# Optimization experiments

Hardware: AMD Instinct MI355X
Metric: run time of the kernel (lower is better)

Reference implementation:

```python
import jax, jax.numpy as jnp
from jax import lax
import numpy as np

DN = ('NDHWC', 'DHWIO', 'NDHWC')

def _conv(x, W):
    # stride-1 kernel-3 sparse conv on dense grid: SAME conv; absent voxels are zero
    return lax.conv_general_dilated(x, W, (1, 1, 1), 'SAME', dimension_numbers=DN)

def _tconv(x, W):
    # kernel-2 stride-2 generative transpose conv: exactly doubles each spatial dim
    return lax.conv_transpose(x, W, (2, 2, 2), 'VALID', dimension_numbers=DN)

def _pool(h):
    B, D1, D2, D3, C = h.shape
    return h.reshape(B, D1 // 2, 2, D2 // 2, 2, D3 // 2, 2, C).max(axis=(2, 4, 6))

def _pool_mask(m):
    B, D1, D2, D3 = m.shape
    return m.reshape(B, D1 // 2, 2, D2 // 2, 2, D3 // 2, 2).max(axis=(2, 4, 6))

def _up_mask(m):
    return jnp.repeat(jnp.repeat(jnp.repeat(m, 2, axis=1), 2, axis=2), 2, axis=3)

def setup_inputs() -> dict:
    key = jax.random.key(0)
    ks = jax.random.split(key, 6)
    B, G = 2, 128
    x = jax.random.normal(ks[0], (B, G, G, G, 1), dtype=jnp.float32)
    occ = jax.random.randint(ks[1], (B, G, G, G), 0, 10, dtype=jnp.int32)
    def xavier(k, shape):
        fan_in = np.prod(shape[:-1]); fan_out = shape[-1]
        std = np.sqrt(2.0 / (fan_in + fan_out)).astype(np.float32)
        return jax.random.normal(k, shape, dtype=jnp.float32) * std
    W1 = xavier(ks[2], (3, 3, 3, 1, 16))
    W2 = xavier(ks[3], (3, 3, 3, 16, 4))
    Wt1 = xavier(ks[4], (2, 2, 2, 4, 16))
    Wt2 = xavier(ks[5], (2, 2, 2, 16, 1))
    return {"x": x, "W1": W1, "W2": W2, "Wt1": Wt1, "Wt2": Wt2, "occ": occ}

def reference(x, W1, W2, Wt1, Wt2, occ):
    m0 = (occ == 0).astype(x.dtype)            # occupancy mask at full res
    xm = x * m0[..., None]
    h = jax.nn.relu(_conv(xm, W1)) * m0[..., None]   # coords unchanged
    h = _pool(h); m1 = _pool_mask(m0)                # stride-2 max pool on sparse coords
    h = jax.nn.relu(_conv(h, W2)) * m1[..., None]
    h = _pool(h); m2 = _pool_mask(m1)
    m3 = _up_mask(m2)                                # transpose conv emits all children coords
    h = jax.nn.relu(_tconv(h, Wt1)) * m3[..., None]
    m4 = _up_mask(m3)
    out = jax.nn.sigmoid(_tconv(h, Wt2)) * m4[..., None]
    return out
```

## Files before the change

### kernel.cpp

```cpp
#include <hip/hip_runtime.h>
#include <hip/hip_fp16.h>

#define G 128

typedef _Float16 h2_t __attribute__((ext_vector_type(2)));

union U16 { uint4 u; h2_t h2[4]; };
union HV  { uint4 u; h2_t h2[4]; };
union PK2 { uint2 u; h2_t h[2]; };

__device__ __forceinline__ float dot2f(h2_t a, h2_t b, float c) {
#if __has_builtin(__builtin_amdgcn_fdot2)
    return __builtin_amdgcn_fdot2(a, b, c, false);
#else
    return c + (float)a.x * (float)b.x + (float)a.y * (float)b.y;
#endif
}

__device__ __forceinline__ float dot4(float4 a, float4 b) {
    return a.x * b.x + a.y * b.y + a.z * b.z + a.w * b.w;
}

__global__ __launch_bounds__(256, 1)
void k_conv1_pool(const float* __restrict__ x, const int* __restrict__ occ,
                  const float* __restrict__ W1,
                  __half* __restrict__ h1p, float* __restrict__ m1)
{
    __shared__ __align__(16) _Float16      sx[10 * 18 * 24];
    __shared__ __align__(16) int           pacc[16 * 256];
    __shared__ __align__(4)  unsigned short slist[2048];
    __shared__ __align__(16) h2_t          w1L[216];
    __shared__ __align__(4)  unsigned char sm1[256];
    __shared__ int                         scnt;

    const int bx = blockIdx.x, by = blockIdx.y;
    const int b  = blockIdx.z >> 4, zt = blockIdx.z & 15;
    const int tid = threadIdx.x;

    const int z0 = zt * 8 - 1, y0 = by * 16 - 1;
    const int base_b = b * G * G * G;

    int4   ro[5];
    float4 rx[5];
    #pragma unroll
    for (int it = 0; it < 5; ++it) {
        int c = it * 256 + tid;
        int cc = c < 1080 ? c : 1079;
        int row = cc / 6, seg = cc - row * 6;
        int lz  = row / 18, ly = row - lz * 18;
        int gz = z0 + lz, gy = y0 + ly;
        int gxc = (bx << 4) - 4 + (seg << 2);
        bool inb = (unsigned)gz < 128u && (unsigned)gy < 128u && (unsigned)gxc < 128u;
        int gi = inb ? base_b + (gz * G + gy) * G + gxc : base_b;
        ro[it] = *(const int4*)(occ + gi);
        rx[it] = *(const float4*)(x + gi);
    }

    if (tid == 0) scnt = 0;
    {
        uint4 z4 = make_uint4(0u, 0u, 0u, 0u);
        uint4* p4 = (uint4*)pacc;
        p4[tid] = z4; p4[tid + 256] = z4; p4[tid + 512] = z4; p4[tid + 768] = z4;
    }
    if (tid < 64) ((unsigned*)sm1)[tid] = 0u;
    if (tid < 216) {
        float2 f = ((const float2*)W1)[tid];
        h2_t w; w.x = (_Float16)f.x; w.y = (_Float16)f.y;
        w1L[tid] = w;
    }
    __syncthreads();

    #pragma unroll
    for (int it = 0; it < 5; ++it) {
        int c = it * 256 + tid;
        if (c < 1080) {
            int row = c / 6, seg = c - row * 6;
            int lz  = row / 18, ly = row - lz * 18;
            int gz = z0 + lz, gy = y0 + ly;
            int gxc = (bx << 4) - 4 + (seg << 2);
            bool inb = (unsigned)gz < 128u && (unsigned)gy < 128u && (unsigned)gxc < 128u;
            int4   o4 = ro[it];
            float4 x4 = rx[it];
            if (!inb) o4 = make_int4(1, 1, 1, 1);
            h2_t p01, p23;
            p01.x = (o4.x == 0) ? (_Float16)x4.x : (_Float16)0.f;
            p01.y = (o4.y == 0) ? (_Float16)x4.y : (_Float16)0.f;
            p23.x = (o4.z == 0) ? (_Float16)x4.z : (_Float16)0.f;
            p23.y = (o4.w == 0) ? (_Float16)x4.w : (_Float16)0.f;
            PK2 pk; pk.h[0] = p01; pk.h[1] = p23;
            *(uint2*)&sx[row * 24 + (seg << 2)] = pk.u;

            if ((unsigned)(lz - 1) < 8u && (unsigned)(ly - 1) < 16u &&
                (unsigned)(seg - 1) < 4u) {
                int mb = (o4.x == 0 ? 1 : 0) | (o4.y == 0 ? 2 : 0) |
                         (o4.z == 0 ? 4 : 0) | (o4.w == 0 ? 8 : 0);
                if (mb) {
                    int cnt  = __popc(mb);
                    int base = atomicAdd(&scnt, cnt);
                    int cz = lz - 1, cy = ly - 1, cx0v = (seg << 2) - 4;
                    int cellb = (cz >> 1) * 64 + (cy >> 1) * 8;
                    #pragma unroll
                    for (int j = 0; j < 4; ++j) {
                        if (mb & (1 << j)) {
                            slist[base++] = (unsigned short)((cz << 8) | (cy << 4) | (cx0v + j));
                            sm1[cellb + ((cx0v + j) >> 1)] = (unsigned char)1;
                        }
                    }
                }
            }
        }
    }
    __syncthreads();

    const int n = scnt;

    const h2_t zero = (h2_t)(_Float16)0.f;
    for (int kb = 0; kb < n; kb += 256) {
        const int idx = kb + tid;
        if (idx < n) {
            const int code = slist[idx];
            const int cz = code >> 8, cy = (code >> 4) & 15, cx = code & 15;
            const int sb = ((cz + 1) * 18 + (cy + 1)) * 24 + cx + 4;
            h2_t acc[8];
            #pragma unroll
            for (int c = 0; c < 8; ++c) acc[c] = zero;
            #pragma unroll
            for (int kz = 0; kz < 3; ++kz)
            #pragma unroll
            for (int ky = 0; ky < 3; ++ky)
            #pragma unroll
            for (int kx = 0; kx < 3; ++kx) {
                _Float16 v = sx[sb + (kz - 1) * 432 + (ky - 1) * 24 + (kx - 1)];
                h2_t v2 = {v, v};
                const h2_t* w = &w1L[((kz * 3 + ky) * 3 + kx) * 8];
                #pragma unroll
                for (int c = 0; c < 8; ++c) acc[c] = v2 * w[c] + acc[c];
            }
            const int cell = (cz >> 1) * 64 + (cy >> 1) * 8 + (cx >> 1);
            #pragma unroll
            for (int c = 0; c < 8; ++c) {
                atomicMax(&pacc[(2 * c) * 256 + cell],
                          __float_as_int(fmaxf((float)acc[c].x, 0.f)));
                atomicMax(&pacc[(2 * c + 1) * 256 + cell],
                          __float_as_int(fmaxf((float)acc[c].y, 0.f)));
            }
        }
    }
    __syncthreads();

    const int tx = tid & 7, ty = (tid >> 3) & 7, tz = tid >> 6;
    const int pz = zt * 4 + tz, py = by * 8 + ty, px = bx * 8 + tx;
    const int vidx = ((b * 64 + pz) * 64 + py) * 64 + px;
    HV p0, p1;
    #pragma unroll
    for (int c = 0; c < 4; ++c) {
        h2_t a, bq;
        a.x  = (_Float16)__int_as_float(pacc[(2 * c) * 256 + tid]);
        a.y  = (_Float16)__int_as_float(pacc[(2 * c + 1) * 256 + tid]);
        bq.x = (_Float16)__int_as_float(pacc[(8 + 2 * c) * 256 + tid]);
        bq.y = (_Float16)__int_as_float(pacc[(9 + 2 * c) * 256 + tid]);
        p0.h2[c] = a; p1.h2[c] = bq;
    }
    uint4* o = (uint4*)&h1p[(size_t)vidx * 16];
    o[0] = p0.u;
    o[1] = p1.u;
    m1[vidx] = sm1[tid] ? 1.f : 0.f;
}

__global__ __launch_bounds__(256)
void k_conv2_dec(const __half* __restrict__ h1p, const float* __restrict__ m1,
                 const float* __restrict__ W2,
                 const float* __restrict__ Wt1, const float* __restrict__ Wt2,
                 float* __restrict__ out)
{
    __shared__ uint4  tile[1320];
    __shared__ float4 wt1[128];
    __shared__ float4 wt2[32];
    __shared__ __align__(16) h2_t w2L[864];
    __shared__ int    pacc[128];
    __shared__ int    pm[32];
    __shared__ unsigned char slist[256];
    __shared__ int    scnt;

    const int bx = blockIdx.x, by = blockIdx.y;
    const int b  = blockIdx.z >> 4, bz = blockIdx.z & 15;
    const int tid = threadIdx.x;

    const int z0 = bz * 4 - 1, y0 = by * 8 - 1, x0 = bx * 8 - 1;

    uint4 ra[3], rb4[3];
    #pragma unroll
    for (int it = 0; it < 3; ++it) {
        int g = it * 256 + tid;
        int gg = g < 660 ? g : 659;
        int z = gg / 110, r = gg - z * 110, y = r / 11, xx = r - y * 11;
        int gz = z0 + z, gy = y0 + y, gx = x0 + xx;
        bool inb = (unsigned)gz < 64u && (unsigned)gy < 64u && (unsigned)gx < 64u;
        size_t vi = inb ? (size_t)(((b * 64 + gz) * 64 + gy) * 64 + gx) : 0;
        const uint4* src = (const uint4*)&h1p[vi * 16];
        ra[it]  = src[0];
        rb4[it] = src[1];
    }

    const int cx_ = tid & 7, cy_ = (tid >> 3) & 7, cz_ = tid >> 6;
    const float mv = m1[((b * 64 + (bz * 4 + cz_)) * 64 + (by * 8 + cy_)) * 64
                        + (bx * 8 + cx_)];

    if (tid == 0) scnt = 0;
    if (tid < 128) { wt1[tid] = ((const float4*)Wt1)[tid]; pacc[tid] = 0; }
    if (tid < 32)  { wt2[tid] = ((const float4*)Wt2)[tid]; pm[tid] = 0; }
    #pragma unroll
    for (int it = 0; it < 4; ++it) {
        int i = it * 256 + tid;
        if (i < 864) {
            int t = i >> 5, rr = i & 31, co = rr >> 3, p = rr & 7;
            h2_t w;
            w.x = (_Float16)W2[t * 64 + (2 * p) * 4 + co];
            w.y = (_Float16)W2[t * 64 + (2 * p + 1) * 4 + co];
            w2L[i] = w;
        }
    }
    __syncthreads();

    #pragma unroll
    for (int it = 0; it < 3; ++it) {
        int g = it * 256 + tid;
        if (g < 660) {
            int z = g / 110, r = g - z * 110, y = r / 11, xx = r - y * 11;
            int gz = z0 + z, gy = y0 + y, gx = x0 + xx;
            bool inb = (unsigned)gz < 64u && (unsigned)gy < 64u && (unsigned)gx < 64u;
            uint4 a0 = ra[it], a1 = rb4[it];
            if (!inb) { a0 = make_uint4(0u, 0u, 0u, 0u); a1 = a0; }
            tile[g]       = a0;
            tile[660 + g] = a1;
        }
    }
    {
        const int lane = tid & 63;
        bool act = (mv != 0.f);
        unsigned long long bal = __ballot(act);
        int wtot = __popcll(bal);
        int wbase = 0;
        if (lane == 0 && wtot) wbase = atomicAdd(&scnt, wtot);
        wbase = __shfl(wbase, 0);
        if (act) {
            int pre = __popcll(bal & ((1ull << lane) - 1ull));
            slist[wbase + pre] = (unsigned char)tid;
            pm[(cz_ >> 1) * 16 + (cy_ >> 1) * 4 + (cx_ >> 1)] = 1;
        }
    }
    __syncthreads();

    const int n = scnt;

    if (tid < n) {
        const int code = slist[tid];
        const int cx = code & 7, cy = (code >> 3) & 7, cz = code >> 6;
        float acc[4] = {0.f, 0.f, 0.f, 0.f};
        #pragma unroll
        for (int kz = 0; kz < 3; ++kz)
        #pragma unroll
        for (int ky = 0; ky < 3; ++ky) {
            const int rb = ((cz + kz) * 10 + (cy + ky)) * 11 + cx;
            h2_t hp[2][3][4];
            #pragma unroll
            for (int hh = 0; hh < 2; ++hh)
            #pragma unroll
            for (int xi = 0; xi < 3; ++xi) {
                U16 a; a.u = tile[hh * 660 + rb + xi];
                #pragma unroll
                for (int p = 0; p < 4; ++p) hp[hh][xi][p] = a.h2[p];
            }
            const int t3 = (kz * 3 + ky) * 3;
            #pragma unroll
            for (int kx = 0; kx < 3; ++kx) {
                const h2_t* w = &w2L[(t3 + kx) * 32];
                #pragma unroll
                for (int co = 0; co < 4; ++co) {
                    float a = acc[co];
                    #pragma unroll
                    for (int hh = 0; hh < 2; ++hh)
                    #pragma unroll
                    for (int p = 0; p < 4; ++p)
                        a = dot2f(hp[hh][kx][p], w[co * 8 + 4 * hh + p], a);
                    acc[co] = a;
                }
            }
        }
        const int parent = (cz >> 1) * 16 + (cy >> 1) * 4 + (cx >> 1);
        #pragma unroll
        for (int co = 0; co < 4; ++co)
            atomicMax(&pacc[co * 32 + parent],
                      __float_as_int(fmaxf(acc[co], 0.f)));
    }
    __syncthreads();

    {
        const int p  = tid >> 3;
        const int a  = (tid >> 2) & 1;
        const int bb = (tid >> 1) & 1;
        const int e  = tid & 1;
        const int pZ = p >> 4, pY = (p >> 2) & 3, pq = p & 3;
        const int pz = bz * 2 + pZ, py = by * 4 + pY, pxq = bx * 4 + pq;

        const float mm = pm[p] ? 1.f : 0.f;
        const float4 hv = make_float4(__int_as_float(pacc[p]),
                                      __int_as_float(pacc[32 + p]),
                                      __int_as_float(pacc[64 + p]),
                                      __int_as_float(pacc[96 + p]));

        const int b0q = ((((1 - a) * 2 + (1 - bb)) * 2) + 1) * 16;
        const int b1q = ((((1 - a) * 2 + (1 - bb)) * 2) + 0) * 16;
        float4 t0q[4], t1q[4];
        #pragma unroll
        for (int q = 0; q < 4; ++q) {
            float4 a0 = wt1[b0q + q],      a1 = wt1[b0q + 4 + q];
            float4 a2 = wt1[b0q + 8 + q],  a3 = wt1[b0q + 12 + q];
            float4 c0 = wt1[b1q + q],      c1 = wt1[b1q + 4 + q];
            float4 c2 = wt1[b1q + 8 + q],  c3 = wt1[b1q + 12 + q];
            float4 s0, s1;
            s0.x = hv.x * a0.x + hv.y * a1.x + hv.z * a2.x + hv.w * a3.x;
            s0.y = hv.x * a0.y + hv.y * a1.y + hv.z * a2.y + hv.w * a3.y;
            s0.z = hv.x * a0.z + hv.y * a1.z + hv.z * a2.z + hv.w * a3.z;
            s0.w = hv.x * a0.w + hv.y * a1.w + hv.z * a2.w + hv.w * a3.w;
            s1.x = hv.x * c0.x + hv.y * c1.x + hv.z * c2.x + hv.w * c3.x;
            s1.y = hv.x * c0.y + hv.y * c1.y + hv.z * c2.y + hv.w * c3.y;
            s1.z = hv.x * c0.z + hv.y * c1.z + hv.z * c2.z + hv.w * c3.z;
            s1.w = hv.x * c0.w + hv.y * c1.w + hv.z * c2.w + hv.w * c3.w;
            t0q[q] = make_float4(fmaxf(s0.x, 0.f), fmaxf(s0.y, 0.f),
                                 fmaxf(s0.z, 0.f), fmaxf(s0.w, 0.f));
            t1q[q] = make_float4(fmaxf(s1.x, 0.f), fmaxf(s1.y, 0.f),
                                 fmaxf(s1.z, 0.f), fmaxf(s1.w, 0.f));
        }

        const int d = 4 * pz + 2 * a + e;
        #pragma unroll
        for (int f = 0; f < 2; ++f) {
            const int hh = 4 * py + 2 * bb + f;
            const int be = ((1 - e) * 2 + (1 - f)) * 2;
            const float4* wg0 = &wt2[(be + 1) * 4];
            const float4* wg1 = &wt2[(be + 0) * 4];
            float s00 = dot4(t0q[0], wg0[0]) + dot4(t0q[1], wg0[1])
                      + dot4(t0q[2], wg0[2]) + dot4(t0q[3], wg0[3]);
            float s01 = dot4(t0q[0], wg1[0]) + dot4(t0q[1], wg1[1])
                      + dot4(t0q[2], wg1[2]) + dot4(t0q[3], wg1[3]);
            float s10 = dot4(t1q[0], wg0[0]) + dot4(t1q[1], wg0[1])
                      + dot4(t1q[2], wg0[2]) + dot4(t1q[3], wg0[3]);
            float s11 = dot4(t1q[0], wg1[0]) + dot4(t1q[1], wg1[1])
                      + dot4(t1q[2], wg1[2]) + dot4(t1q[3], wg1[3]);
            float4 o;
            o.x = mm / (1.f + __expf(-s00));
            o.y = mm / (1.f + __expf(-s01));
            o.z = mm / (1.f + __expf(-s10));
            o.w = mm / (1.f + __expf(-s11));
            *(float4*)&out[((b * G + d) * G + hh) * G + 4 * pxq] = o;
        }
    }
}

extern "C" void kernel_launch(void* const* d_in, const int* in_sizes, int n_in,
                              void* d_out, int out_size, void* d_ws, size_t ws_size,
                              hipStream_t stream) {
    (void)in_sizes; (void)n_in; (void)out_size; (void)ws_size;
    const float* x   = (const float*)d_in[0];
    const float* W1  = (const float*)d_in[1];
    const float* W2  = (const float*)d_in[2];
    const float* Wt1 = (const float*)d_in[3];
    const float* Wt2 = (const float*)d_in[4];
    const int*   occ = (const int*)d_in[5];
    float* out = (float*)d_out;

    char* ws = (char*)d_ws;
    __half* h1p = (__half*)ws;
    float*  m1  = (float*)(ws + 8388608ull * sizeof(__half));

    k_conv1_pool<<<dim3(8, 8, 32), dim3(256), 0, stream>>>(x, occ, W1, h1p, m1);
    k_conv2_dec<<<dim3(8, 8, 32), dim3(256), 0, stream>>>(h1p, m1, W2, Wt1, Wt2, out);
}
```

Before: 152.5 us.

## Gather conv2 neighbors directly from global memory and swizzle block order

Drops the shared-memory halo tile in the conv2/decoder kernel. Each active voxel now reads its 27 neighbor feature vectors straight from global memory, with a one-row software prefetch (double-buffered registers). Because only about 10% of voxels are active, this avoids loading and staging the full 660-voxel halo per block and frees LDS for higher occupancy. It also remaps the block index to a swizzled work order, likely to improve cache locality. The cost is redundant global and L2 traffic between neighboring active voxels, plus more register pressure from the prefetch buffers.

```diff
diff --git a/kernel.cpp b/kernel.cpp
--- a/kernel.cpp
+++ b/kernel.cpp
@@ -173,7 +173,6 @@
                  const float* __restrict__ Wt1, const float* __restrict__ Wt2,
                  float* __restrict__ out)
 {
-    __shared__ uint4  tile[1320];
     __shared__ float4 wt1[128];
     __shared__ float4 wt2[32];
     __shared__ __align__(16) h2_t w2L[864];
@@ -182,25 +181,13 @@
     __shared__ unsigned char slist[256];
     __shared__ int    scnt;
 
-    const int bx = blockIdx.x, by = blockIdx.y;
-    const int b  = blockIdx.z >> 4, bz = blockIdx.z & 15;
     const int tid = threadIdx.x;
 
-    const int z0 = bz * 4 - 1, y0 = by * 8 - 1, x0 = bx * 8 - 1;
-
-    uint4 ra[3], rb4[3];
-    #pragma unroll
-    for (int it = 0; it < 3; ++it) {
-        int g = it * 256 + tid;
-        int gg = g < 660 ? g : 659;
-        int z = gg / 110, r = gg - z * 110, y = r / 11, xx = r - y * 11;
-        int gz = z0 + z, gy = y0 + y, gx = x0 + xx;
-        bool inb = (unsigned)gz < 64u && (unsigned)gy < 64u && (unsigned)gx < 64u;
-        size_t vi = inb ? (size_t)(((b * 64 + gz) * 64 + gy) * 64 + gx) : 0;
-        const uint4* src = (const uint4*)&h1p[vi * 16];
-        ra[it]  = src[0];
-        rb4[it] = src[1];
-    }
+    const int lin  = blockIdx.x + 8 * (blockIdx.y + 8 * blockIdx.z);
+    const int wrk  = ((lin & 7) << 8) | (lin >> 3);
+    const int bx   = wrk & 7, by = (wrk >> 3) & 7;
+    const int zidx = wrk >> 6;
+    const int b    = zidx >> 4, bz = zidx & 15;
 
     const int cx_ = tid & 7, cy_ = (tid >> 3) & 7, cz_ = tid >> 6;
     const float mv = m1[((b * 64 + (bz * 4 + cz_)) * 64 + (by * 8 + cy_)) * 64
@@ -222,19 +209,6 @@
     }
     __syncthreads();
 
-    #pragma unroll
-    for (int it = 0; it < 3; ++it) {
-        int g = it * 256 + tid;
-        if (g < 660) {
-            int z = g / 110, r = g - z * 110, y = r / 11, xx = r - y * 11;
-            int gz = z0 + z, gy = y0 + y, gx = x0 + xx;
-            bool inb = (unsigned)gz < 64u && (unsigned)gy < 64u && (unsigned)gx < 64u;
-            uint4 a0 = ra[it], a1 = rb4[it];
-            if (!inb) { a0 = make_uint4(0u, 0u, 0u, 0u); a1 = a0; }
-            tile[g]       = a0;
-            tile[660 + g] = a1;
-        }
-    }
     {
         const int lane = tid & 63;
         bool act = (mv != 0.f);
@@ -256,37 +230,77 @@
     if (tid < n) {
         const int code = slist[tid];
         const int cx = code & 7, cy = (code >> 3) & 7, cz = code >> 6;
+        const int gz0 = bz * 4 + cz - 1;
+        const int gy0 = by * 8 + cy - 1;
+        const int gx0 = bx * 8 + cx - 1;
+        const __half* __restrict__ hb = h1p + ((size_t)b << 18) * 16;
+
         float acc[4] = {0.f, 0.f, 0.f, 0.f};
+
+        uint4 curv[3][2], nxtv[3][2];
+
+        {
+            const int gz = gz0, gy = gy0;
+            const bool zy = ((unsigned)gz < 64u) && ((unsigned)gy < 64u);
+            #pragma unroll
+            for (int xi = 0; xi < 3; ++xi) {
+                const int gx = gx0 + xi;
+                const bool ok = zy && ((unsigned)gx < 64u);
+                const size_t vi = ok ? (size_t)((gz * 64 + gy) * 64 + gx) : 0;
+                const uint4* s = (const uint4*)&hb[vi * 16];
+                uint4 a0 = s[0], a1 = s[1];
+                if (!ok) { a0 = make_uint4(0u,0u,0u,0u); a1 = a0; }
+                curv[xi][0] = a0; curv[xi][1] = a1;
+            }
+        }
+
         #pragma unroll
-        for (int kz = 0; kz < 3; ++kz)
-        #pragma unroll
-        for (int ky = 0; ky < 3; ++ky) {
-            const int rb = ((cz + kz) * 10 + (cy + ky)) * 11 + cx;
-            h2_t hp[2][3][4];
-            #pragma unroll
-            for (int hh = 0; hh < 2; ++hh)
-            #pragma unroll
-            for (int xi = 0; xi < 3; ++xi) {
-                U16 a; a.u = tile[hh * 660 + rb + xi];
+        for (int r = 0; r < 9; ++r) {
+            if (r < 8) {
+                const int rz = (r + 1) / 3, ry = (r + 1) - rz * 3;
+                const int gz = gz0 + rz, gy = gy0 + ry;
+                const bool zy = ((unsigned)gz < 64u) && ((unsigned)gy < 64u);
                 #pragma unroll
-                for (int p = 0; p < 4; ++p) hp[hh][xi][p] = a.h2[p];
-            }
-            const int t3 = (kz * 3 + ky) * 3;
-            #pragma unroll
-            for (int kx = 0; kx < 3; ++kx) {
-                const h2_t* w = &w2L[(t3 + kx) * 32];
+                for (int xi = 0; xi < 3; ++xi) {
+                    const int gx = gx0 + xi;
+                    const bool ok = zy && ((unsigned)gx < 64u);
+                    const size_t vi = ok ? (size_t)((gz * 64 + gy) * 64 + gx) : 0;
+                    const uint4* s = (const uint4*)&hb[vi * 16];
+                    uint4 a0 = s[0], a1 = s[1];
+                    if (!ok) { a0 = make_uint4(0u,0u,0u,0u); a1 = a0; }
+                    nxtv[xi][0] = a0; nxtv[xi][1] = a1;
+                }
+            }
+
+            {
+                const h2_t* wrow = &w2L[(r * 3) * 32];
                 #pragma unroll
-                for (int co = 0; co < 4; ++co) {
-                    float a = acc[co];
+                for (int kx = 0; kx < 3; ++kx) {
+                    U16 a0; a0.u = curv[kx][0];
+                    U16 a1; a1.u = curv[kx][1];
+                    const h2_t* wv = wrow + kx * 32;
                     #pragma unroll
-                    for (int hh = 0; hh < 2; ++hh)
-                    #pragma unroll
-                    for (int p = 0; p < 4; ++p)
-                        a = dot2f(hp[hh][kx][p], w[co * 8 + 4 * hh + p], a);
-                    acc[co] = a;
+                    for (int co = 0; co < 4; ++co) {
+                        float a = acc[co];
+                        #pragma unroll
+                        for (int p = 0; p < 4; ++p) {
+                            a = dot2f(a0.h2[p], wv[co * 8 + p], a);
+                            a = dot2f(a1.h2[p], wv[co * 8 + 4 + p], a);
+                        }
+                        acc[co] = a;
+                    }
                 }
             }
-        }
+
+            if (r < 8) {
+                #pragma unroll
+                for (int xi = 0; xi < 3; ++xi) {
+                    curv[xi][0] = nxtv[xi][0];
+                    curv[xi][1] = nxtv[xi][1];
+                }
+            }
+        }
+
         const int parent = (cz >> 1) * 16 + (cy >> 1) * 4 + (cx >> 1);
         #pragma unroll
         for (int co = 0; co < 4; ++co)
```

Result: no change. 151.0 us (-1.0%).

## Fuse conv1+pool into conv2/decoder kernel, recomputing halo per block

Applied to the files above, without the earlier changes.

Merges the two kernels into one, so the pooled conv1 feature map is no longer written to and read back from global workspace. Each block now loads a larger occ/x halo and computes conv1 densely per pooled cell, with register max-pooling instead of a sparse list and shared atomics. It also shrinks the output tile to one pooled z-slab and remaps block indices for locality. The cost is redundant halo recomputation of conv1 and dense work on unoccupied voxels, which are skipped only per voxel by a mask bit.

```diff
diff --git a/kernel.cpp b/kernel.cpp
--- a/kernel.cpp
+++ b/kernel.cpp
@@ -17,39 +17,62 @@
 #endif
 }
 
+__device__ __forceinline__ h2_t h2max(h2_t a, h2_t b) {
+#if __has_builtin(__builtin_elementwise_max)
+    return __builtin_elementwise_max(a, b);
+#else
+    h2_t r;
+    r.x = a.x > b.x ? a.x : b.x;
+    r.y = a.y > b.y ? a.y : b.y;
+    return r;
+#endif
+}
+
 __device__ __forceinline__ float dot4(float4 a, float4 b) {
     return a.x * b.x + a.y * b.y + a.z * b.z + a.w * b.w;
 }
 
-__global__ __launch_bounds__(256, 1)
-void k_conv1_pool(const float* __restrict__ x, const int* __restrict__ occ,
-                  const float* __restrict__ W1,
-                  __half* __restrict__ h1p, float* __restrict__ m1)
+__global__ __launch_bounds__(256)
+void k_fused(const float* __restrict__ x, const int* __restrict__ occ,
+             const float* __restrict__ W1, const float* __restrict__ W2,
+             const float* __restrict__ Wt1, const float* __restrict__ Wt2,
+             float* __restrict__ out)
 {
-    __shared__ __align__(16) _Float16      sx[10 * 18 * 24];
-    __shared__ __align__(16) int           pacc[16 * 256];
-    __shared__ __align__(4)  unsigned short slist[2048];
+    __shared__ __align__(16) _Float16      sx[10 * 22 * 24];
+    __shared__ __align__(4)  unsigned char mk[10 * 22 * 6];
+    __shared__ __align__(16) uint4         tile[2 * 400];
+    __shared__ unsigned char               sm1L[400];
     __shared__ __align__(16) h2_t          w1L[216];
-    __shared__ __align__(4)  unsigned char sm1[256];
+    __shared__ __align__(16) h2_t          w2L[864];
+    __shared__ float4                      wt1[128];
+    __shared__ float4                      wt2[32];
+    __shared__ int                         pacc[64];
+    __shared__ int                         pm[16];
+    __shared__ unsigned char               clist[128];
     __shared__ int                         scnt;
 
-    const int bx = blockIdx.x, by = blockIdx.y;
-    const int b  = blockIdx.z >> 4, zt = blockIdx.z & 15;
     const int tid = threadIdx.x;
 
-    const int z0 = zt * 8 - 1, y0 = by * 16 - 1;
+    const int lin = blockIdx.x + 8 * (blockIdx.y + 8 * blockIdx.z);
+    const int wrk = ((lin & 7) << 9) | (lin >> 3);
+    const int bx  = wrk & 7, by = (wrk >> 3) & 7;
+    const int bzz = wrk >> 6;
+    const int b   = bzz >> 5, bz2 = bzz & 31;
+
     const int base_b = b * G * G * G;
-
-    int4   ro[5];
-    float4 rx[5];
+    const int gz0 = 4 * bz2 - 3;
+    const int gy0 = 16 * by - 3;
+    const int gx0 = 16 * bx - 4;
+
+    int4   ro[6];
+    float4 rx[6];
     #pragma unroll
-    for (int it = 0; it < 5; ++it) {
+    for (int it = 0; it < 6; ++it) {
         int c = it * 256 + tid;
-        int cc = c < 1080 ? c : 1079;
+        int cc = c < 1320 ? c : 1319;
         int row = cc / 6, seg = cc - row * 6;
-        int lz  = row / 18, ly = row - lz * 18;
-        int gz = z0 + lz, gy = y0 + ly;
-        int gxc = (bx << 4) - 4 + (seg << 2);
+        int lz = row / 22, ly = row - lz * 22;
+        int gz = gz0 + lz, gy = gy0 + ly, gxc = gx0 + (seg << 2);
         bool inb = (unsigned)gz < 128u && (unsigned)gy < 128u && (unsigned)gxc < 128u;
         int gi = inb ? base_b + (gz * G + gy) * G + gxc : base_b;
         ro[it] = *(const int4*)(occ + gi);
@@ -57,27 +80,34 @@
     }
 
     if (tid == 0) scnt = 0;
-    {
-        uint4 z4 = make_uint4(0u, 0u, 0u, 0u);
-        uint4* p4 = (uint4*)pacc;
-        p4[tid] = z4; p4[tid + 256] = z4; p4[tid + 512] = z4; p4[tid + 768] = z4;
-    }
-    if (tid < 64) ((unsigned*)sm1)[tid] = 0u;
+    if (tid < 64) pacc[tid] = 0;
+    if (tid < 16) pm[tid] = 0;
+    if (tid < 128) wt1[tid] = ((const float4*)Wt1)[tid];
+    if (tid < 32)  wt2[tid] = ((const float4*)Wt2)[tid];
     if (tid < 216) {
         float2 f = ((const float2*)W1)[tid];
         h2_t w; w.x = (_Float16)f.x; w.y = (_Float16)f.y;
         w1L[tid] = w;
     }
-    __syncthreads();
-
     #pragma unroll
-    for (int it = 0; it < 5; ++it) {
+    for (int it = 0; it < 4; ++it) {
+        int i = it * 256 + tid;
+        if (i < 864) {
+            int t = i >> 5, rr = i & 31, co = rr >> 3, p = rr & 7;
+            h2_t w;
+            w.x = (_Float16)W2[t * 64 + (2 * p) * 4 + co];
+            w.y = (_Float16)W2[t * 64 + (2 * p + 1) * 4 + co];
+            w2L[i] = w;
+        }
+    }
+
+    #pragma unroll
+    for (int it = 0; it < 6; ++it) {
         int c = it * 256 + tid;
-        if (c < 1080) {
+        if (c < 1320) {
             int row = c / 6, seg = c - row * 6;
-            int lz  = row / 18, ly = row - lz * 18;
-            int gz = z0 + lz, gy = y0 + ly;
-            int gxc = (bx << 4) - 4 + (seg << 2);
+            int lz = row / 22, ly = row - lz * 22;
+            int gz = gz0 + lz, gy = gy0 + ly, gxc = gx0 + (seg << 2);
             bool inb = (unsigned)gz < 128u && (unsigned)gy < 128u && (unsigned)gxc < 128u;
             int4   o4 = ro[it];
             float4 x4 = rx[it];
@@ -89,155 +119,89 @@
             p23.y = (o4.w == 0) ? (_Float16)x4.w : (_Float16)0.f;
             PK2 pk; pk.h[0] = p01; pk.h[1] = p23;
             *(uint2*)&sx[row * 24 + (seg << 2)] = pk.u;
-
-            if ((unsigned)(lz - 1) < 8u && (unsigned)(ly - 1) < 16u &&
-                (unsigned)(seg - 1) < 4u) {
-                int mb = (o4.x == 0 ? 1 : 0) | (o4.y == 0 ? 2 : 0) |
-                         (o4.z == 0 ? 4 : 0) | (o4.w == 0 ? 8 : 0);
-                if (mb) {
-                    int cnt  = __popc(mb);
-                    int base = atomicAdd(&scnt, cnt);
-                    int cz = lz - 1, cy = ly - 1, cx0v = (seg << 2) - 4;
-                    int cellb = (cz >> 1) * 64 + (cy >> 1) * 8;
+            mk[c] = (unsigned char)((o4.x == 0 ? 1 : 0) | (o4.y == 0 ? 2 : 0) |
+                                    (o4.z == 0 ? 4 : 0) | (o4.w == 0 ? 8 : 0));
+        }
+    }
+    __syncthreads();
+
+    {
+        const h2_t zero = (h2_t)(_Float16)0.f;
+        const h2_t* sxh2 = (const h2_t*)sx;
+        #pragma unroll
+        for (int pass = 0; pass < 2; ++pass) {
+            int t = pass * 256 + tid;
+            if (t < 400) {
+                const int tz = t / 100, rm = t - tz * 100;
+                const int ty = rm / 10,  tx = rm - ty * 10;
+
+                h2_t cube[4][4][3];
+                #pragma unroll
+                for (int z4 = 0; z4 < 4; ++z4) {
+                    const int lz = 2 * tz + z4;
                     #pragma unroll
-                    for (int j = 0; j < 4; ++j) {
-                        if (mb & (1 << j)) {
-                            slist[base++] = (unsigned short)((cz << 8) | (cy << 4) | (cx0v + j));
-                            sm1[cellb + ((cx0v + j) >> 1)] = (unsigned char)1;
-                        }
+                    for (int y4 = 0; y4 < 4; ++y4) {
+                        const int base = (lz * 22 + 2 * ty + y4) * 12 + tx;
+                        cube[z4][y4][0] = sxh2[base];
+                        cube[z4][y4][1] = sxh2[base + 1];
+                        cube[z4][y4][2] = sxh2[base + 2];
                     }
                 }
+
+                h2_t best[8];
+                #pragma unroll
+                for (int c = 0; c < 8; ++c) best[c] = zero;
+                int anym = 0;
+
+                #pragma unroll
+                for (int pos = 0; pos < 8; ++pos) {
+                    const int dz = pos >> 2, dy = (pos >> 1) & 1, dx = pos & 1;
+                    const int lz = 1 + 2 * tz + dz;
+                    const int ly = 1 + 2 * ty + dy;
+                    const int lx = 2 + 2 * tx + dx;
+                    const int mbit = (mk[(lz * 22 + ly) * 6 + (lx >> 2)] >> (lx & 3)) & 1;
+                    if (mbit) {
+                        anym = 1;
+                        h2_t acc[8];
+                        #pragma unroll
+                        for (int c = 0; c < 8; ++c) acc[c] = zero;
+                        #pragma unroll
+                        for (int kz = 0; kz < 3; ++kz)
+                        #pragma unroll
+                        for (int ky = 0; ky < 3; ++ky)
+                        #pragma unroll
+                        for (int kx = 0; kx < 3; ++kx) {
+                            const int xp = dx + kx + 1;
+                            h2_t cv = cube[dz + kz][dy + ky][xp >> 1];
+                            _Float16 v = (xp & 1) ? cv.y : cv.x;
+                            h2_t v2 = {v, v};
+                            const h2_t* w = &w1L[((kz * 3 + ky) * 3 + kx) * 8];
+                            #pragma unroll
+                            for (int c = 0; c < 8; ++c) acc[c] = v2 * w[c] + acc[c];
+                        }
+                        #pragma unroll
+                        for (int c = 0; c < 8; ++c)
+                            best[c] = h2max(best[c], h2max(acc[c], zero));
+                    }
+                }
+
+                HV p0, p1;
+                #pragma unroll
+                for (int c = 0; c < 4; ++c) { p0.h2[c] = best[c]; p1.h2[c] = best[4 + c]; }
+                tile[t]       = p0.u;
+                tile[400 + t] = p1.u;
+                sm1L[t] = (unsigned char)anym;
             }
         }
     }
     __syncthreads();
 
-    const int n = scnt;
-
-    const h2_t zero = (h2_t)(_Float16)0.f;
-    for (int kb = 0; kb < n; kb += 256) {
-        const int idx = kb + tid;
-        if (idx < n) {
-            const int code = slist[idx];
-            const int cz = code >> 8, cy = (code >> 4) & 15, cx = code & 15;
-            const int sb = ((cz + 1) * 18 + (cy + 1)) * 24 + cx + 4;
-            h2_t acc[8];
-            #pragma unroll
-            for (int c = 0; c < 8; ++c) acc[c] = zero;
-            #pragma unroll
-            for (int kz = 0; kz < 3; ++kz)
-            #pragma unroll
-            for (int ky = 0; ky < 3; ++ky)
-            #pragma unroll
-            for (int kx = 0; kx < 3; ++kx) {
-                _Float16 v = sx[sb + (kz - 1) * 432 + (ky - 1) * 24 + (kx - 1)];
-                h2_t v2 = {v, v};
-                const h2_t* w = &w1L[((kz * 3 + ky) * 3 + kx) * 8];
-                #pragma unroll
-                for (int c = 0; c < 8; ++c) acc[c] = v2 * w[c] + acc[c];
-            }
-            const int cell = (cz >> 1) * 64 + (cy >> 1) * 8 + (cx >> 1);
-            #pragma unroll
-            for (int c = 0; c < 8; ++c) {
-                atomicMax(&pacc[(2 * c) * 256 + cell],
-                          __float_as_int(fmaxf((float)acc[c].x, 0.f)));
-                atomicMax(&pacc[(2 * c + 1) * 256 + cell],
-                          __float_as_int(fmaxf((float)acc[c].y, 0.f)));
-            }
-        }
-    }
-    __syncthreads();
-
-    const int tx = tid & 7, ty = (tid >> 3) & 7, tz = tid >> 6;
-    const int pz = zt * 4 + tz, py = by * 8 + ty, px = bx * 8 + tx;
-    const int vidx = ((b * 64 + pz) * 64 + py) * 64 + px;
-    HV p0, p1;
-    #pragma unroll
-    for (int c = 0; c < 4; ++c) {
-        h2_t a, bq;
-        a.x  = (_Float16)__int_as_float(pacc[(2 * c) * 256 + tid]);
-        a.y  = (_Float16)__int_as_float(pacc[(2 * c + 1) * 256 + tid]);
-        bq.x = (_Float16)__int_as_float(pacc[(8 + 2 * c) * 256 + tid]);
-        bq.y = (_Float16)__int_as_float(pacc[(9 + 2 * c) * 256 + tid]);
-        p0.h2[c] = a; p1.h2[c] = bq;
-    }
-    uint4* o = (uint4*)&h1p[(size_t)vidx * 16];
-    o[0] = p0.u;
-    o[1] = p1.u;
-    m1[vidx] = sm1[tid] ? 1.f : 0.f;
-}
-
-__global__ __launch_bounds__(256)
-void k_conv2_dec(const __half* __restrict__ h1p, const float* __restrict__ m1,
-                 const float* __restrict__ W2,
-                 const float* __restrict__ Wt1, const float* __restrict__ Wt2,
-                 float* __restrict__ out)
-{
-    __shared__ uint4  tile[1320];
-    __shared__ float4 wt1[128];
-    __shared__ float4 wt2[32];
-    __shared__ __align__(16) h2_t w2L[864];
-    __shared__ int    pacc[128];
-    __shared__ int    pm[32];
-    __shared__ unsigned char slist[256];
-    __shared__ int    scnt;
-
-    const int bx = blockIdx.x, by = blockIdx.y;
-    const int b  = blockIdx.z >> 4, bz = blockIdx.z & 15;
-    const int tid = threadIdx.x;
-
-    const int z0 = bz * 4 - 1, y0 = by * 8 - 1, x0 = bx * 8 - 1;
-
-    uint4 ra[3], rb4[3];
-    #pragma unroll
-    for (int it = 0; it < 3; ++it) {
-        int g = it * 256 + tid;
-        int gg = g < 660 ? g : 659;
-        int z = gg / 110, r = gg - z * 110, y = r / 11, xx = r - y * 11;
-        int gz = z0 + z, gy = y0 + y, gx = x0 + xx;
-        bool inb = (unsigned)gz < 64u && (unsigned)gy < 64u && (unsigned)gx < 64u;
-        size_t vi = inb ? (size_t)(((b * 64 + gz) * 64 + gy) * 64 + gx) : 0;
-        const uint4* src = (const uint4*)&h1p[vi * 16];
-        ra[it]  = src[0];
-        rb4[it] = src[1];
-    }
-
-    const int cx_ = tid & 7, cy_ = (tid >> 3) & 7, cz_ = tid >> 6;
-    const float mv = m1[((b * 64 + (bz * 4 + cz_)) * 64 + (by * 8 + cy_)) * 64
-                        + (bx * 8 + cx_)];
-
-    if (tid == 0) scnt = 0;
-    if (tid < 128) { wt1[tid] = ((const float4*)Wt1)[tid]; pacc[tid] = 0; }
-    if (tid < 32)  { wt2[tid] = ((const float4*)Wt2)[tid]; pm[tid] = 0; }
-    #pragma unroll
-    for (int it = 0; it < 4; ++it) {
-        int i = it * 256 + tid;
-        if (i < 864) {
-            int t = i >> 5, rr = i & 31, co = rr >> 3, p = rr & 7;
-            h2_t w;
-            w.x = (_Float16)W2[t * 64 + (2 * p) * 4 + co];
-            w.y = (_Float16)W2[t * 64 + (2 * p + 1) * 4 + co];
-            w2L[i] = w;
-        }
-    }
-    __syncthreads();
-
-    #pragma unroll
-    for (int it = 0; it < 3; ++it) {
-        int g = it * 256 + tid;
-        if (g < 660) {
-            int z = g / 110, r = g - z * 110, y = r / 11, xx = r - y * 11;
-            int gz = z0 + z, gy = y0 + y, gx = x0 + xx;
-            bool inb = (unsigned)gz < 64u && (unsigned)gy < 64u && (unsigned)gx < 64u;
-            uint4 a0 = ra[it], a1 = rb4[it];
-            if (!inb) { a0 = make_uint4(0u, 0u, 0u, 0u); a1 = a0; }
-            tile[g]       = a0;
-            tile[660 + g] = a1;
-        }
-    }
     {
+        const int ox = tid & 7, oy = (tid >> 3) & 7, oz = tid >> 6;
+        bool act = false;
+        if (tid < 128)
+            act = sm1L[((oz + 1) * 10 + oy + 1) * 10 + ox + 1] != 0;
         const int lane = tid & 63;
-        bool act = (mv != 0.f);
         unsigned long long bal = __ballot(act);
         int wtot = __popcll(bal);
         int wbase = 0;
@@ -245,8 +209,8 @@
         wbase = __shfl(wbase, 0);
         if (act) {
             int pre = __popcll(bal & ((1ull << lane) - 1ull));
-            slist[wbase + pre] = (unsigned char)tid;
-            pm[(cz_ >> 1) * 16 + (cy_ >> 1) * 4 + (cx_ >> 1)] = 1;
+            clist[wbase + pre] = (unsigned char)tid;
+            pm[(oy >> 1) * 4 + (ox >> 1)] = 1;
         }
     }
     __syncthreads();
@@ -254,20 +218,20 @@
     const int n = scnt;
 
     if (tid < n) {
-        const int code = slist[tid];
-        const int cx = code & 7, cy = (code >> 3) & 7, cz = code >> 6;
+        const int code = clist[tid];
+        const int ox = code & 7, oy = (code >> 3) & 7, oz = code >> 6;
         float acc[4] = {0.f, 0.f, 0.f, 0.f};
         #pragma unroll
         for (int kz = 0; kz < 3; ++kz)
         #pragma unroll
         for (int ky = 0; ky < 3; ++ky) {
-            const int rb = ((cz + kz) * 10 + (cy + ky)) * 11 + cx;
+            const int rb = ((oz + kz) * 10 + (oy + ky)) * 10 + ox;
             h2_t hp[2][3][4];
             #pragma unroll
             for (int hh = 0; hh < 2; ++hh)
             #pragma unroll
             for (int xi = 0; xi < 3; ++xi) {
-                U16 a; a.u = tile[hh * 660 + rb + xi];
+                U16 a; a.u = tile[hh * 400 + rb + xi];
                 #pragma unroll
                 for (int p = 0; p < 4; ++p) hp[hh][xi][p] = a.h2[p];
             }
@@ -287,27 +251,28 @@
                 }
             }
         }
-        const int parent = (cz >> 1) * 16 + (cy >> 1) * 4 + (cx >> 1);
+        const int parent = (oy >> 1) * 4 + (ox >> 1);
         #pragma unroll
         for (int co = 0; co < 4; ++co)
-            atomicMax(&pacc[co * 32 + parent],
+            atomicMax(&pacc[co * 16 + parent],
                       __float_as_int(fmaxf(acc[co], 0.f)));
     }
     __syncthreads();
 
     {
-        const int p  = tid >> 3;
-        const int a  = (tid >> 2) & 1;
-        const int bb = (tid >> 1) & 1;
-        const int e  = tid & 1;
-        const int pZ = p >> 4, pY = (p >> 2) & 3, pq = p & 3;
-        const int pz = bz * 2 + pZ, py = by * 4 + pY, pxq = bx * 4 + pq;
+        const int p  = tid >> 4;
+        const int a  = (tid >> 3) & 1;
+        const int bb = (tid >> 2) & 1;
+        const int e  = (tid >> 1) & 1;
+        const int f  = tid & 1;
+        const int pY = p >> 2, pq = p & 3;
+        const int py = by * 4 + pY, pxq = bx * 4 + pq;
 
         const float mm = pm[p] ? 1.f : 0.f;
         const float4 hv = make_float4(__int_as_float(pacc[p]),
+                                      __int_as_float(pacc[16 + p]),
                                       __int_as_float(pacc[32 + p]),
-                                      __int_as_float(pacc[64 + p]),
-                                      __int_as_float(pacc[96 + p]));
+                                      __int_as_float(pacc[48 + p]));
 
         const int b0q = ((((1 - a) * 2 + (1 - bb)) * 2) + 1) * 16;
         const int b1q = ((((1 - a) * 2 + (1 - bb)) * 2) + 0) * 16;
@@ -333,35 +298,32 @@
                                  fmaxf(s1.z, 0.f), fmaxf(s1.w, 0.f));
         }
 
-        const int d = 4 * pz + 2 * a + e;
-        #pragma unroll
-        for (int f = 0; f < 2; ++f) {
-            const int hh = 4 * py + 2 * bb + f;
-            const int be = ((1 - e) * 2 + (1 - f)) * 2;
-            const float4* wg0 = &wt2[(be + 1) * 4];
-            const float4* wg1 = &wt2[(be + 0) * 4];
-            float s00 = dot4(t0q[0], wg0[0]) + dot4(t0q[1], wg0[1])
-                      + dot4(t0q[2], wg0[2]) + dot4(t0q[3], wg0[3]);
-            float s01 = dot4(t0q[0], wg1[0]) + dot4(t0q[1], wg1[1])
-                      + dot4(t0q[2], wg1[2]) + dot4(t0q[3], wg1[3]);
-            float s10 = dot4(t1q[0], wg0[0]) + dot4(t1q[1], wg0[1])
-                      + dot4(t1q[2], wg0[2]) + dot4(t1q[3], wg0[3]);
-            float s11 = dot4(t1q[0], wg1[0]) + dot4(t1q[1], wg1[1])
-                      + dot4(t1q[2], wg1[2]) + dot4(t1q[3], wg1[3]);
-            float4 o;
-            o.x = mm / (1.f + __expf(-s00));
-            o.y = mm / (1.f + __expf(-s01));
-            o.z = mm / (1.f + __expf(-s10));
-            o.w = mm / (1.f + __expf(-s11));
-            *(float4*)&out[((b * G + d) * G + hh) * G + 4 * pxq] = o;
-        }
+        const int d  = 4 * bz2 + 2 * a + e;
+        const int hh = 4 * py + 2 * bb + f;
+        const int be = ((1 - e) * 2 + (1 - f)) * 2;
+        const float4* wg0 = &wt2[(be + 1) * 4];
+        const float4* wg1 = &wt2[(be + 0) * 4];
+        float s00 = dot4(t0q[0], wg0[0]) + dot4(t0q[1], wg0[1])
+                  + dot4(t0q[2], wg0[2]) + dot4(t0q[3], wg0[3]);
+        float s01 = dot4(t0q[0], wg1[0]) + dot4(t0q[1], wg1[1])
+                  + dot4(t0q[2], wg1[2]) + dot4(t0q[3], wg1[3]);
+        float s10 = dot4(t1q[0], wg0[0]) + dot4(t1q[1], wg0[1])
+                  + dot4(t1q[2], wg0[2]) + dot4(t1q[3], wg0[3]);
+        float s11 = dot4(t1q[0], wg1[0]) + dot4(t1q[1], wg1[1])
+                  + dot4(t1q[2], wg1[2]) + dot4(t1q[3], wg1[3]);
+        float4 o;
+        o.x = mm / (1.f + __expf(-s00));
+        o.y = mm / (1.f + __expf(-s01));
+        o.z = mm / (1.f + __expf(-s10));
+        o.w = mm / (1.f + __expf(-s11));
+        *(float4*)&out[((b * G + d) * G + hh) * G + 4 * pxq] = o;
     }
 }
 
 extern "C" void kernel_launch(void* const* d_in, const int* in_sizes, int n_in,
                               void* d_out, int out_size, void* d_ws, size_t ws_size,
                               hipStream_t stream) {
-    (void)in_sizes; (void)n_in; (void)out_size; (void)ws_size;
+    (void)in_sizes; (void)n_in; (void)out_size; (void)d_ws; (void)ws_size;
     const float* x   = (const float*)d_in[0];
     const float* W1  = (const float*)d_in[1];
     const float* W2  = (const float*)d_in[2];
@@ -370,10 +332,5 @@
     const int*   occ = (const int*)d_in[5];
     float* out = (float*)d_out;
 
-    char* ws = (char*)d_ws;
-    __half* h1p = (__half*)ws;
-    float*  m1  = (float*)(ws + 8388608ull * sizeof(__half));
-
-    k_conv1_pool<<<dim3(8, 8, 32), dim3(256), 0, stream>>>(x, occ, W1, h1p, m1);
-    k_conv2_dec<<<dim3(8, 8, 32), dim3(256), 0, stream>>>(h1p, m1, W2, Wt1, Wt2, out);
-}
+    k_fused<<<dim3(8, 8, 64), dim3(256), 0, stream>>>(x, occ, W1, W2, Wt1, Wt2, out);
+}
```

Result: slower. 248.3 us (+62.9%).
